# Performance work log

Measured on AMD Instinct MI355X. Metric: run time of the kernel, lower is better.

Reference implementation:

```python
import jax, jax.numpy as jnp
import numpy as np

N, DIM, HID, NCLS, E = 100000, 256, 16, 64, 3200000
NEG_SLOPE = 0.2


def setup_inputs() -> dict:
    key = jax.random.key(0)
    ks = jax.random.split(key, 10)
    x = jax.random.normal(ks[0], (N, DIM), dtype=jnp.float32)
    edge_index = jax.random.randint(ks[1], (2, E), 0, N, dtype=jnp.int64)
    # GATConv params (heads=1): glorot-ish scaled normals
    W1 = jax.random.normal(ks[2], (DIM, HID), dtype=jnp.float32) / np.sqrt(DIM)
    a_src1 = jax.random.normal(ks[3], (HID,), dtype=jnp.float32) / np.sqrt(HID)
    a_dst1 = jax.random.normal(ks[4], (HID,), dtype=jnp.float32) / np.sqrt(HID)
    b1 = jnp.zeros((HID,), dtype=jnp.float32)
    W2 = jax.random.normal(ks[5], (HID, NCLS), dtype=jnp.float32) / np.sqrt(HID)
    a_src2 = jax.random.normal(ks[6], (NCLS,), dtype=jnp.float32) / np.sqrt(NCLS)
    a_dst2 = jax.random.normal(ks[7], (NCLS,), dtype=jnp.float32) / np.sqrt(NCLS)
    b2 = jnp.zeros((NCLS,), dtype=jnp.float32)
    return {"x": x, "edge_index": edge_index, "W1": W1, "a_src1": a_src1,
            "a_dst1": a_dst1, "b1": b1, "W2": W2, "a_src2": a_src2,
            "a_dst2": a_dst2, "b2": b2}


def gat_conv(x, src, dst, W, a_s, a_d, b, n):
    # PyG GATConv, heads=1: h = x W; e_ij = LeakyReLU(a_s.h_j + a_d.h_i)
    h = x @ W                                   # [N, out]
    alpha_s = h @ a_s                           # [N]
    alpha_d = h @ a_d                           # [N]
    e = jax.nn.leaky_relu(alpha_s[src] + alpha_d[dst], NEG_SLOPE)  # [E]
    # softmax over edges grouped by destination node
    m = jax.ops.segment_max(e, dst, num_segments=n)
    m = jnp.where(jnp.isfinite(m), m, 0.0)
    ee = jnp.exp(e - m[dst])
    denom = jax.ops.segment_sum(ee, dst, num_segments=n)
    alpha = ee / denom[dst]                     # self-loops guarantee denom > 0
    out = jax.ops.segment_sum(h[src] * alpha[:, None], dst, num_segments=n)
    return out + b


def reference(x, edge_index, W1, a_src1, a_dst1, b1, W2, a_src2, a_dst2, b2):
    n = x.shape[0]
    loop = jnp.arange(n, dtype=edge_index.dtype)
    src = jnp.concatenate([edge_index[0], loop])  # add self-loops (PyG default)
    dst = jnp.concatenate([edge_index[1], loop])
    h = jax.nn.relu(gat_conv(x, src, dst, W1, a_src1, a_dst1, b1, n))
    # F.dropout treated as identity (inference / deterministic reference)
    out = gat_conv(h, src, dst, W2, a_src2, a_dst2, b2, n)
    return jax.nn.log_softmax(out, axis=1)
```

## Files before the change

kernel.cpp:

```cpp
#include <hip/hip_runtime.h>
#include <hip/hip_fp16.h>


#define DIM 256
#define HID 16
#define NCLS 64
#define NEG 0.2f
#define P1_CHUNK 4096
#define KITER 16
#define CAP 8704

typedef _Float16 f16x8 __attribute__((ext_vector_type(8)));
typedef float f32x4 __attribute__((ext_vector_type(4)));

__device__ __forceinline__ float lrelu(float v) { return v >= 0.f ? v : NEG * v; }

__device__ __forceinline__ uint4 pack_half8(const float* v) {
    __half2 p0 = __floats2half2_rn(v[0], v[1]);
    __half2 p1 = __floats2half2_rn(v[2], v[3]);
    __half2 p2 = __floats2half2_rn(v[4], v[5]);
    __half2 p3 = __floats2half2_rn(v[6], v[7]);
    return make_uint4(*(unsigned*)&p0, *(unsigned*)&p1, *(unsigned*)&p2, *(unsigned*)&p3);
}

__device__ __forceinline__ void unpack_half8(uint4 u, float* f) {
    float2 f0 = __half22float2(*(__half2*)&u.x);
    float2 f1 = __half22float2(*(__half2*)&u.y);
    float2 f2 = __half22float2(*(__half2*)&u.z);
    float2 f3 = __half22float2(*(__half2*)&u.w);
    f[0] = f0.x; f[1] = f0.y; f[2] = f1.x; f[3] = f1.y;
    f[4] = f2.x; f[5] = f2.y; f[6] = f3.x; f[7] = f3.y;
}

__global__ void vsd_kernel(const float* __restrict__ W2, const float* __restrict__ as2,
                           const float* __restrict__ ad2, float* __restrict__ vsd,
                           int* __restrict__ bkt_cnt, int* __restrict__ bkt_cur, int capb) {
    int t = threadIdx.x;
    bkt_cnt[t] = 0;
    bkt_cur[t] = capb ? t * capb : 0;
    if (t < 32) {
        int j = t & 15;
        const float* a = (t < 16) ? as2 : ad2;
        float s = 0.f;
        for (int c = 0; c < NCLS; ++c) s += W2[j * NCLS + c] * a[c];
        vsd[t] = s;
    }
}


__global__ __launch_bounds__(256) void p0_hist(const int* __restrict__ dst, int E,
                                               int* __restrict__ bkt_cnt) {
    __shared__ int hist[512];
    int t = threadIdx.x;
    for (int i = t; i < 512; i += 256) hist[i] = 0;
    __syncthreads();
    int base = blockIdx.x * P1_CHUNK;
#pragma unroll
    for (int k = 0; k < KITER; ++k) {
        int idx = base + k * 256 + t;
        if (idx < E) atomicAdd(&hist[dst[idx] >> 8], 1);
    }
    __syncthreads();
    for (int i = t; i < 512; i += 256)
        if (hist[i]) atomicAdd(&bkt_cnt[i], hist[i]);
}

__global__ void scanb(int* __restrict__ bkt_cnt, int* __restrict__ bkt_cur,
                      int* __restrict__ bkt_base, int nb) {
    __shared__ int lds[512];
    int t = threadIdx.x;
    int v = (t < nb) ? bkt_cnt[t] : 0;
    lds[t] = v;
    __syncthreads();
    for (int o = 1; o < 512; o <<= 1) {
        int x = (t >= o) ? lds[t - o] : 0;
        __syncthreads();
        lds[t] += x;
        __syncthreads();
    }
    if (t < nb) {
        int e = lds[t] - v;
        bkt_base[t] = e;
        bkt_cur[t] = e;
    }
}

struct H1S {
    _Float16 w1t[16][264];
    _Float16 hst[4][16][16];
};

__global__ __launch_bounds__(256) void p1h1_kernel(
    const int* __restrict__ ei, int E, int* __restrict__ bkt_cur,
    int* __restrict__ coarse, int nS, int h1blk, int capb,
    const float* __restrict__ x, const float* __restrict__ W1,
    uint4* __restrict__ h1h, int n) {
    __shared__ union __align__(16) { int hist[512]; H1S h1; } sm;
    int t = threadIdx.x;
    int bid = blockIdx.x;
    int total = nS + h1blk;
    int f0 = (int)(((long long)bid * h1blk) / total);
    int f1 = (int)(((long long)(bid + 1) * h1blk) / total);
    if (f1 == f0) {
        int sb = bid - f0;
        int base = sb * P1_CHUNK;
        int sarr[KITER], darr[KITER];
        for (int i = t; i < 512; i += 256) sm.hist[i] = 0;
        bool e4 = ((E & 3) == 0);
#pragma unroll
        for (int k = 0; k < KITER / 4; ++k) {
            int idx = base + (k * 256 + t) * 4;
            if (e4 && idx + 3 < E) {
                int4 s4 = *(const int4*)&ei[idx];
                int4 d4 = *(const int4*)&ei[E + idx];
                sarr[4 * k] = s4.x; sarr[4 * k + 1] = s4.y;
                sarr[4 * k + 2] = s4.z; sarr[4 * k + 3] = s4.w;
                darr[4 * k] = d4.x; darr[4 * k + 1] = d4.y;
                darr[4 * k + 2] = d4.z; darr[4 * k + 3] = d4.w;
            } else {
#pragma unroll
                for (int j = 0; j < 4; ++j) {
                    int id2 = idx + j;
                    if (id2 < E) { sarr[4 * k + j] = ei[id2]; darr[4 * k + j] = ei[E + id2]; }
                    else darr[4 * k + j] = -1;
                }
            }
        }
        __syncthreads();
#pragma unroll
        for (int k = 0; k < KITER; ++k)
            if (darr[k] >= 0) atomicAdd(&sm.hist[darr[k] >> 8], 1);
        __syncthreads();
        for (int b = t; b < 512; b += 256) {
            int c = sm.hist[b];
            sm.hist[b] = c ? atomicAdd(&bkt_cur[b], c) : 0;
        }
        __syncthreads();
#pragma unroll
        for (int k = 0; k < KITER; ++k) {
            int d = darr[k];
            if (d >= 0) {
                int bk = d >> 8;
                int pos = atomicAdd(&sm.hist[bk], 1);
                if (capb) pos = min(pos, (bk + 1) * capb - 1);
                coarse[pos] = (sarr[k] << 8) | (d & 255);
            }
        }
    } else {
        int hb = f0;
        {
            const float* row = W1 + t * HID;
#pragma unroll
            for (int nn2 = 0; nn2 < 16; ++nn2)
                sm.h1.w1t[nn2][t] = (_Float16)row[nn2];
        }
        __syncthreads();
        int lane = t & 63, wave = t >> 6;
        int q = lane >> 4, nn = lane & 15;
#pragma unroll 1
        for (int it = 0; it < 4; ++it) {
            int nb = hb * 256 + wave * 64 + it * 16;
            int node = nb + nn;
            const float* xr = x + (size_t)min(node, n - 1) * DIM;
            float4 st[16];
#pragma unroll
            for (int s = 0; s < 8; ++s) {
                int kb = s * 32 + q * 8;
                st[2 * s]     = *(const float4*)(xr + kb);
                st[2 * s + 1] = *(const float4*)(xr + kb + 4);
            }
            f32x4 acc = {0.f, 0.f, 0.f, 0.f};
#pragma unroll
            for (int s = 0; s < 8; ++s) {
                int kb = s * 32 + q * 8;
                f16x8 bf = *(const f16x8*)&sm.h1.w1t[nn][kb];
                float4 a0 = st[2 * s], a1 = st[2 * s + 1];
                f16x8 af;
                af[0] = (_Float16)a0.x; af[1] = (_Float16)a0.y;
                af[2] = (_Float16)a0.z; af[3] = (_Float16)a0.w;
                af[4] = (_Float16)a1.x; af[5] = (_Float16)a1.y;
                af[6] = (_Float16)a1.z; af[7] = (_Float16)a1.w;
                acc = __builtin_amdgcn_mfma_f32_16x16x32_f16(af, bf, acc, 0, 0, 0);
            }
            if (nb < n) {
#pragma unroll
                for (int r = 0; r < 4; ++r)
                    sm.h1.hst[wave][q * 4 + r][nn] = (_Float16)acc[r];
                __builtin_amdgcn_s_waitcnt(0);
                if (lane < 32) {
                    int nl = lane >> 1, jq = lane & 1;
                    int nd = nb + nl;
                    if (nd < n)
                        h1h[(size_t)nd * 2 + jq] = *(const uint4*)&sm.h1.hst[wave][nl][jq * 8];
                }
            }
        }
    }
}

__global__ __launch_bounds__(512) void p2_fine(const int* __restrict__ coarse,
                                               const int* __restrict__ bkt_base,
                                               const int* __restrict__ bkt_cnt,
                                               const int* __restrict__ bkt_cur,
                                               int* __restrict__ csr, int* __restrict__ row_ptr,
                                               int* __restrict__ deg, int n, int capb) {
    __shared__ int cnt[256];
    __shared__ int off[256];
    __shared__ int csr_loc[CAP];
    int b = blockIdx.x;
    int t = threadIdx.x;
    int m, wbase;
    if (capb) {
        int* sc = csr_loc;
        int cv = bkt_cur[t] - t * capb;
        sc[t] = cv;
        __syncthreads();
        for (int o = 1; o < 512; o <<= 1) {
            int xg = (t >= o) ? sc[t - o] : 0;
            __syncthreads();
            sc[t] += xg;
            __syncthreads();
        }
        m = bkt_cur[b] - b * capb;
        wbase = sc[b] - m;
        __syncthreads();
    } else {
        m = bkt_cnt[b];
        wbase = bkt_base[b];
    }
    int rbase = capb ? b * capb : wbase;
    if (t < 256) cnt[t] = 0;
    __syncthreads();
    for (int i = t; i < m; i += 512) atomicAdd(&cnt[coarse[rbase + i] & 255], 1);
    __syncthreads();
    int v = 0;
    if (t < 256) { v = cnt[t]; off[t] = v; }
    __syncthreads();
    for (int o = 1; o < 256; o <<= 1) {
        int xg = (t >= o && t < 256) ? off[t - o] : 0;
        __syncthreads();
        if (t < 256) off[t] += xg;
        __syncthreads();
    }
    if (t < 256) {
        int excl = off[t] - v;
        int node = b * 256 + t;
        if (node < n) {
            row_ptr[node] = wbase + excl;
            deg[node] = v;
        }
        cnt[t] = excl;
    }
    __syncthreads();
    if (m <= CAP) {
        for (int i = t; i < m; i += 512) {
            int rec = coarse[rbase + i];
            int pos = atomicAdd(&cnt[rec & 255], 1);
            csr_loc[pos] = rec >> 8;
        }
        __syncthreads();
        for (int i = t; i < m; i += 512) csr[wbase + i] = csr_loc[i];
    } else {
        for (int i = t; i < m; i += 512) {
            int rec = coarse[rbase + i];
            int pos = atomicAdd(&cnt[rec & 255], 1);
            csr[wbase + pos] = rec >> 8;
        }
    }
}


__device__ __forceinline__ void agg_core(
    const uint4* __restrict__ hh, const float* aw, const float* dw,
    int node, int start, int cnt, const int* __restrict__ csr,
    int lg, int eq, int jq, int gbase, float* acc, float* hs, float& denomv) {
    unpack_half8(hh[(size_t)node * 2 + jq], hs);
    float asn = 0.f, adn = 0.f;
#pragma unroll
    for (int i = 0; i < 8; ++i) { asn += hs[i] * aw[i]; adn += hs[i] * dw[i]; }
    asn += __shfl_xor(asn, 1, 64);
    adn += __shfl_xor(adn, 1, 64);
    float adi = adn;
    float w0 = __expf(lrelu(asn + adi));
    float w0s = (eq == 0) ? w0 : 0.f;
#pragma unroll
    for (int i = 0; i < 8; ++i) acc[i] = w0s * hs[i];
    float denom = w0s;
    int svA = (lg < cnt) ? csr[start + lg] : 0;
    int svB = (16 + lg < cnt) ? csr[start + 16 + lg] : 0;
#pragma unroll 1
    for (int q0 = 0; q0 < cnt; q0 += 32) {
        int nA = q0 + 32 + lg, nB = q0 + 48 + lg;
        int nsvA = (nA < cnt) ? csr[start + nA] : 0;
        int nsvB = (nB < cnt) ? csr[start + nB] : 0;
        int sl0 = gbase + eq, sl1 = gbase + 8 + eq;
        int s0 = __shfl(svA, sl0, 64);
        int s1 = __shfl(svA, sl1, 64);
        int s2 = __shfl(svB, sl0, 64);
        int s3 = __shfl(svB, sl1, 64);
        uint4 u0 = hh[(size_t)s0 * 2 + jq];
        uint4 u1 = hh[(size_t)s1 * 2 + jq];
        uint4 u2 = hh[(size_t)s2 * 2 + jq];
        uint4 u3 = hh[(size_t)s3 * 2 + jq];
        float h0[8], h1v[8], h2[8], h3[8];
        unpack_half8(u0, h0);
        unpack_half8(u1, h1v);
        unpack_half8(u2, h2);
        unpack_half8(u3, h3);
        float p0 = 0.f, p1 = 0.f, p2 = 0.f, p3 = 0.f;
#pragma unroll
        for (int i = 0; i < 8; ++i) {
            p0 += h0[i] * aw[i];
            p1 += h1v[i] * aw[i];
            p2 += h2[i] * aw[i];
            p3 += h3[i] * aw[i];
        }
        p0 += __shfl_xor(p0, 1, 64);
        p1 += __shfl_xor(p1, 1, 64);
        p2 += __shfl_xor(p2, 1, 64);
        p3 += __shfl_xor(p3, 1, 64);
        float wA = (q0 + eq < cnt)      ? __expf(lrelu(p0 + adi)) : 0.f;
        float wB = (q0 + 8 + eq < cnt)  ? __expf(lrelu(p1 + adi)) : 0.f;
        float wC = (q0 + 16 + eq < cnt) ? __expf(lrelu(p2 + adi)) : 0.f;
        float wD = (q0 + 24 + eq < cnt) ? __expf(lrelu(p3 + adi)) : 0.f;
        denom += wA + wB + wC + wD;
#pragma unroll
        for (int i = 0; i < 8; ++i)
            acc[i] += wA * h0[i] + wB * h1v[i] + wC * h2[i] + wD * h3[i];
        svA = nsvA;
        svB = nsvB;
    }
#pragma unroll
    for (int m = 2; m <= 8; m <<= 1) {
#pragma unroll
        for (int i = 0; i < 8; ++i) acc[i] += __shfl_xor(acc[i], m, 64);
        denom += __shfl_xor(denom, m, 64);
    }
    denomv = denom;
}

__global__ __launch_bounds__(256) void agg1_kernel(
    const uint4* __restrict__ hh,
    const int* __restrict__ row_ptr, const int* __restrict__ deg, const int* __restrict__ csr,
    const float* __restrict__ as1, const float* __restrict__ ad1,
    const float* __restrict__ bias, uint4* __restrict__ outh, int n) {
    int t = threadIdx.x;
    int node = blockIdx.x * 16 + (t >> 4);
    if (node >= n) return;
    int lg = t & 15, jq = lg & 1, eq = lg >> 1, gbase = t & 48;
    float aw[8], dw[8];
#pragma unroll
    for (int i = 0; i < 8; ++i) { aw[i] = as1[jq * 8 + i]; dw[i] = ad1[jq * 8 + i]; }
    float acc[8], hs[8];
    float denom;
    agg_core(hh, aw, dw, node, row_ptr[node], deg[node], csr, lg, eq, jq, gbase, acc, hs, denom);
    float inv = 1.f / denom;
    float val[8];
#pragma unroll
    for (int i = 0; i < 8; ++i) val[i] = fmaxf(acc[i] * inv + bias[jq * 8 + i], 0.f);
    if (eq == 0) outh[(size_t)node * 2 + jq] = pack_half8(val);
}

__global__ __launch_bounds__(256) void agg2_final_kernel(
    const uint4* __restrict__ hh,
    const int* __restrict__ row_ptr, const int* __restrict__ deg, const int* __restrict__ csr,
    const float* __restrict__ vsd,
    const float* __restrict__ W2, const float* __restrict__ b2,
    float* __restrict__ out, int n) {
    __shared__ float a2s[16 * HID];
    __shared__ float w2s[HID * NCLS];
    __shared__ float b2s[NCLS];
    int t = threadIdx.x;
    for (int i = t; i < HID * NCLS; i += 256) w2s[i] = W2[i];
    if (t < NCLS) b2s[t] = b2[t];
    int g = t >> 4;
    int node = blockIdx.x * 16 + g;
    int lg = t & 15, jq = lg & 1, eq = lg >> 1, gbase = t & 48;
    if (node < n) {
        float aw[8], dw[8];
#pragma unroll
        for (int i = 0; i < 8; ++i) { aw[i] = vsd[jq * 8 + i]; dw[i] = vsd[16 + jq * 8 + i]; }
        float acc[8], hs[8];
        float denom;
        agg_core(hh, aw, dw, node, row_ptr[node], deg[node], csr, lg, eq, jq, gbase, acc, hs, denom);
        float inv = 1.f / denom;
        if (eq == 0) {
            float* dst = &a2s[g * HID + jq * 8];
            *(float4*)dst = make_float4(acc[0] * inv, acc[1] * inv, acc[2] * inv, acc[3] * inv);
            *(float4*)(dst + 4) = make_float4(acc[4] * inv, acc[5] * inv, acc[6] * inv, acc[7] * inv);
        }
    }
    __syncthreads();
    int wv = t >> 6;
    int c = t & 63;
#pragma unroll
    for (int i = 0; i < 4; ++i) {
        int nl = i * 4 + wv;
        int gn = blockIdx.x * 16 + nl;
        if (gn >= n) continue;
        const float* ar = &a2s[nl * HID];
        float v = b2s[c];
#pragma unroll
        for (int j = 0; j < HID; ++j) v += ar[j] * w2s[j * NCLS + c];
        float mx = v;
#pragma unroll
        for (int off = 1; off < 64; off <<= 1) mx = fmaxf(mx, __shfl_xor(mx, off, 64));
        float ex = __expf(v - mx);
        float s = ex;
#pragma unroll
        for (int off = 1; off < 64; off <<= 1) s += __shfl_xor(s, off, 64);
        out[(size_t)gn * NCLS + c] = (v - mx) - __logf(s);
    }
}

extern "C" void kernel_launch(void* const* d_in, const int* in_sizes, int n_in,
                              void* d_out, int out_size, void* d_ws, size_t ws_size,
                              hipStream_t stream) {
    const float* x    = (const float*)d_in[0];
    const int*   ei   = (const int*)d_in[1];
    const float* W1   = (const float*)d_in[2];
    const float* a_s1 = (const float*)d_in[3];
    const float* a_d1 = (const float*)d_in[4];
    const float* b1   = (const float*)d_in[5];
    const float* W2   = (const float*)d_in[6];
    const float* a_s2 = (const float*)d_in[7];
    const float* a_d2 = (const float*)d_in[8];
    const float* b2   = (const float*)d_in[9];
    float* out = (float*)d_out;

    const int N = in_sizes[0] / DIM;
    const int E = in_sizes[1] / 2;
    const int NB = (N + 255) >> 8;
    const int nS = (E + P1_CHUNK - 1) / P1_CHUNK;
    const int h1blk = (N + 255) / 256;

    char* p = (char*)d_ws;
    auto alloc = [&](size_t bytes) {
        char* r = p;
        p += (bytes + 255) & ~(size_t)255;
        return r;
    };
    int*   bkt_cnt  = (int*)alloc(512 * 4);
    int*   bkt_base = (int*)alloc(512 * 4);
    int*   bkt_cur  = (int*)alloc(512 * 4);
    int*   csr      = (int*)alloc((size_t)E * 4);
    int*   row_ptr  = (int*)alloc((size_t)N * 4);
    int*   deg      = (int*)alloc((size_t)N * 4);
    float* vsd      = (float*)alloc(32 * 4);
    uint4* h1h      = (uint4*)alloc((size_t)N * 32);
    uint4* hreluh   = (uint4*)alloc((size_t)N * 32);

    int capb = 10240;
    size_t used = (size_t)(p - (char*)d_ws);
    size_t pad_bytes = (size_t)512 * capb * 4;
    int* coarse;
    if (ws_size - used >= pad_bytes) {
        coarse = (int*)alloc(pad_bytes);
    } else {
        capb = 0;
        coarse = (int*)alloc((size_t)E * 4);
    }

    vsd_kernel<<<1, 512, 0, stream>>>(W2, a_s2, a_d2, vsd, bkt_cnt, bkt_cur, capb);
    if (!capb) {
        p0_hist<<<nS, 256, 0, stream>>>(ei + E, E, bkt_cnt);
        scanb<<<1, 512, 0, stream>>>(bkt_cnt, bkt_cur, bkt_base, NB);
    }
    p1h1_kernel<<<nS + h1blk, 256, 0, stream>>>(ei, E, bkt_cur, coarse, nS, h1blk, capb,
                                                x, W1, h1h, N);
    p2_fine<<<NB, 512, 0, stream>>>(coarse, bkt_base, bkt_cnt, bkt_cur,
                                    csr, row_ptr, deg, N, capb);
    agg1_kernel<<<(N + 15) / 16, 256, 0, stream>>>(h1h, row_ptr, deg, csr,
                                                   a_s1, a_d1, b1, hreluh, N);
    agg2_final_kernel<<<(N + 15) / 16, 256, 0, stream>>>(hreluh, row_ptr, deg, csr,
                                                         vsd, W2, b2, out, N);
}
```

Measured before the change: 299.8 us.

## Drop fine CSR build; aggregate edges per coarse bucket with shared-memory atomics

Removes the p2_fine pass that turned coarse 256-node buckets into a full CSR. Instead, each 512-thread block walks its bucket's edge list directly and accumulates softmax-weighted neighbour features and denominators into shared memory with atomics. It skips the per-node max subtraction and adds the self-loop term at the end. This saves one kernel and the CSR write/read traffic, but uses only about 391 blocks, depends heavily on LDS float atomics (17 per edge), and drops the max-stabilisation, so exp could overflow on other inputs.

```diff
diff --git a/kernel.cpp b/kernel.cpp
--- a/kernel.cpp
+++ b/kernel.cpp
@@ -8,7 +8,6 @@
 #define NEG 0.2f
 #define P1_CHUNK 4096
 #define KITER 16
-#define CAP 8704
 
 typedef _Float16 f16x8 __attribute__((ext_vector_type(8)));
 typedef float f32x4 __attribute__((ext_vector_type(4)));
@@ -30,6 +29,13 @@
     float2 f3 = __half22float2(*(__half2*)&u.w);
     f[0] = f0.x; f[1] = f0.y; f[2] = f1.x; f[3] = f1.y;
     f[4] = f2.x; f[5] = f2.y; f[6] = f3.x; f[7] = f3.y;
+}
+
+__device__ __forceinline__ void unpack_row(const uint4* __restrict__ hh, int s, float* h) {
+    uint4 u0 = hh[(size_t)s * 2];
+    uint4 u1 = hh[(size_t)s * 2 + 1];
+    unpack_half8(u0, h);
+    unpack_half8(u1, h + 8);
 }
 
 __global__ void vsd_kernel(const float* __restrict__ W2, const float* __restrict__ as2,
@@ -198,218 +204,215 @@
     }
 }
 
-__global__ __launch_bounds__(512) void p2_fine(const int* __restrict__ coarse,
-                                               const int* __restrict__ bkt_base,
-                                               const int* __restrict__ bkt_cnt,
-                                               const int* __restrict__ bkt_cur,
-                                               int* __restrict__ csr, int* __restrict__ row_ptr,
-                                               int* __restrict__ deg, int n, int capb) {
-    __shared__ int cnt[256];
-    __shared__ int off[256];
-    __shared__ int csr_loc[CAP];
+
+__global__ __launch_bounds__(512) void agg1_edge_kernel(
+    const int* __restrict__ coarse, const int* __restrict__ bkt_base,
+    const int* __restrict__ bkt_cnt, const int* __restrict__ bkt_cur, int capb,
+    const uint4* __restrict__ hh, const float* __restrict__ a_s1,
+    const float* __restrict__ a_d1, const float* __restrict__ b1,
+    uint4* __restrict__ outh, int n) {
+    __shared__ float acc[256][17];
+    __shared__ float denom[256];
+    __shared__ float asl[256];
+    __shared__ float adl[256];
+    __shared__ float aswv[16], adwv[16], b1s[16];
     int b = blockIdx.x;
     int t = threadIdx.x;
-    int m, wbase;
-    if (capb) {
-        int* sc = csr_loc;
-        int cv = bkt_cur[t] - t * capb;
-        sc[t] = cv;
-        __syncthreads();
-        for (int o = 1; o < 512; o <<= 1) {
-            int xg = (t >= o) ? sc[t - o] : 0;
-            __syncthreads();
-            sc[t] += xg;
-            __syncthreads();
-        }
-        m = bkt_cur[b] - b * capb;
-        wbase = sc[b] - m;
-        __syncthreads();
-    } else {
-        m = bkt_cnt[b];
-        wbase = bkt_base[b];
-    }
-    int rbase = capb ? b * capb : wbase;
-    if (t < 256) cnt[t] = 0;
-    __syncthreads();
-    for (int i = t; i < m; i += 512) atomicAdd(&cnt[coarse[rbase + i] & 255], 1);
-    __syncthreads();
-    int v = 0;
-    if (t < 256) { v = cnt[t]; off[t] = v; }
-    __syncthreads();
-    for (int o = 1; o < 256; o <<= 1) {
-        int xg = (t >= o && t < 256) ? off[t - o] : 0;
-        __syncthreads();
-        if (t < 256) off[t] += xg;
-        __syncthreads();
-    }
+    if (t < 16) { aswv[t] = a_s1[t]; adwv[t] = a_d1[t]; b1s[t] = b1[t]; }
+    for (int i = t; i < 256 * 17; i += 512) ((float*)acc)[i] = 0.f;
+    if (t < 256) denom[t] = 0.f;
+    __syncthreads();
     if (t < 256) {
-        int excl = off[t] - v;
+        int node = b * 256 + t;
+        float s1 = 0.f, s2 = 0.f;
+        if (node < n) {
+            float h[16];
+            unpack_row(hh, node, h);
+#pragma unroll
+            for (int j = 0; j < 16; ++j) { s1 += h[j] * aswv[j]; s2 += h[j] * adwv[j]; }
+        }
+        asl[t] = s1;
+        adl[t] = s2;
+    }
+    __syncthreads();
+    int rb, m;
+    if (capb) { rb = b * capb; m = bkt_cur[b] - rb; }
+    else { rb = bkt_base[b]; m = bkt_cnt[b]; }
+    int i = t;
+    while (i + 512 < m) {
+        int r0 = coarse[rb + i];
+        int r1 = coarse[rb + i + 512];
+        int s0 = r0 >> 8, d0 = r0 & 255;
+        int s1v = r1 >> 8, d1v = r1 & 255;
+        float h0[16], h1[16];
+        unpack_row(hh, s0, h0);
+        unpack_row(hh, s1v, h1);
+        float p0 = 0.f, p1 = 0.f;
+#pragma unroll
+        for (int j = 0; j < 16; ++j) { p0 += h0[j] * aswv[j]; p1 += h1[j] * aswv[j]; }
+        float w0 = __expf(lrelu(p0 + adl[d0]));
+        float w1 = __expf(lrelu(p1 + adl[d1v]));
+#pragma unroll
+        for (int j = 0; j < 16; ++j) {
+            atomicAdd(&acc[d0][j], w0 * h0[j]);
+            atomicAdd(&acc[d1v][j], w1 * h1[j]);
+        }
+        atomicAdd(&denom[d0], w0);
+        atomicAdd(&denom[d1v], w1);
+        i += 1024;
+    }
+    while (i < m) {
+        int r0 = coarse[rb + i];
+        int s0 = r0 >> 8, d0 = r0 & 255;
+        float h0[16];
+        unpack_row(hh, s0, h0);
+        float p0 = 0.f;
+#pragma unroll
+        for (int j = 0; j < 16; ++j) p0 += h0[j] * aswv[j];
+        float w0 = __expf(lrelu(p0 + adl[d0]));
+#pragma unroll
+        for (int j = 0; j < 16; ++j) atomicAdd(&acc[d0][j], w0 * h0[j]);
+        atomicAdd(&denom[d0], w0);
+        i += 512;
+    }
+    __syncthreads();
+    if (t < 256) {
         int node = b * 256 + t;
         if (node < n) {
-            row_ptr[node] = wbase + excl;
-            deg[node] = v;
-        }
-        cnt[t] = excl;
-    }
-    __syncthreads();
-    if (m <= CAP) {
-        for (int i = t; i < m; i += 512) {
-            int rec = coarse[rbase + i];
-            int pos = atomicAdd(&cnt[rec & 255], 1);
-            csr_loc[pos] = rec >> 8;
-        }
-        __syncthreads();
-        for (int i = t; i < m; i += 512) csr[wbase + i] = csr_loc[i];
-    } else {
-        for (int i = t; i < m; i += 512) {
-            int rec = coarse[rbase + i];
-            int pos = atomicAdd(&cnt[rec & 255], 1);
-            csr[wbase + pos] = rec >> 8;
-        }
-    }
-}
-
-
-__device__ __forceinline__ void agg_core(
-    const uint4* __restrict__ hh, const float* aw, const float* dw,
-    int node, int start, int cnt, const int* __restrict__ csr,
-    int lg, int eq, int jq, int gbase, float* acc, float* hs, float& denomv) {
-    unpack_half8(hh[(size_t)node * 2 + jq], hs);
-    float asn = 0.f, adn = 0.f;
-#pragma unroll
-    for (int i = 0; i < 8; ++i) { asn += hs[i] * aw[i]; adn += hs[i] * dw[i]; }
-    asn += __shfl_xor(asn, 1, 64);
-    adn += __shfl_xor(adn, 1, 64);
-    float adi = adn;
-    float w0 = __expf(lrelu(asn + adi));
-    float w0s = (eq == 0) ? w0 : 0.f;
-#pragma unroll
-    for (int i = 0; i < 8; ++i) acc[i] = w0s * hs[i];
-    float denom = w0s;
-    int svA = (lg < cnt) ? csr[start + lg] : 0;
-    int svB = (16 + lg < cnt) ? csr[start + 16 + lg] : 0;
-#pragma unroll 1
-    for (int q0 = 0; q0 < cnt; q0 += 32) {
-        int nA = q0 + 32 + lg, nB = q0 + 48 + lg;
-        int nsvA = (nA < cnt) ? csr[start + nA] : 0;
-        int nsvB = (nB < cnt) ? csr[start + nB] : 0;
-        int sl0 = gbase + eq, sl1 = gbase + 8 + eq;
-        int s0 = __shfl(svA, sl0, 64);
-        int s1 = __shfl(svA, sl1, 64);
-        int s2 = __shfl(svB, sl0, 64);
-        int s3 = __shfl(svB, sl1, 64);
-        uint4 u0 = hh[(size_t)s0 * 2 + jq];
-        uint4 u1 = hh[(size_t)s1 * 2 + jq];
-        uint4 u2 = hh[(size_t)s2 * 2 + jq];
-        uint4 u3 = hh[(size_t)s3 * 2 + jq];
-        float h0[8], h1v[8], h2[8], h3[8];
-        unpack_half8(u0, h0);
-        unpack_half8(u1, h1v);
-        unpack_half8(u2, h2);
-        unpack_half8(u3, h3);
-        float p0 = 0.f, p1 = 0.f, p2 = 0.f, p3 = 0.f;
-#pragma unroll
-        for (int i = 0; i < 8; ++i) {
-            p0 += h0[i] * aw[i];
-            p1 += h1v[i] * aw[i];
-            p2 += h2[i] * aw[i];
-            p3 += h3[i] * aw[i];
-        }
-        p0 += __shfl_xor(p0, 1, 64);
-        p1 += __shfl_xor(p1, 1, 64);
-        p2 += __shfl_xor(p2, 1, 64);
-        p3 += __shfl_xor(p3, 1, 64);
-        float wA = (q0 + eq < cnt)      ? __expf(lrelu(p0 + adi)) : 0.f;
-        float wB = (q0 + 8 + eq < cnt)  ? __expf(lrelu(p1 + adi)) : 0.f;
-        float wC = (q0 + 16 + eq < cnt) ? __expf(lrelu(p2 + adi)) : 0.f;
-        float wD = (q0 + 24 + eq < cnt) ? __expf(lrelu(p3 + adi)) : 0.f;
-        denom += wA + wB + wC + wD;
-#pragma unroll
-        for (int i = 0; i < 8; ++i)
-            acc[i] += wA * h0[i] + wB * h1v[i] + wC * h2[i] + wD * h3[i];
-        svA = nsvA;
-        svB = nsvB;
-    }
-#pragma unroll
-    for (int m = 2; m <= 8; m <<= 1) {
-#pragma unroll
-        for (int i = 0; i < 8; ++i) acc[i] += __shfl_xor(acc[i], m, 64);
-        denom += __shfl_xor(denom, m, 64);
-    }
-    denomv = denom;
-}
-
-__global__ __launch_bounds__(256) void agg1_kernel(
-    const uint4* __restrict__ hh,
-    const int* __restrict__ row_ptr, const int* __restrict__ deg, const int* __restrict__ csr,
-    const float* __restrict__ as1, const float* __restrict__ ad1,
-    const float* __restrict__ bias, uint4* __restrict__ outh, int n) {
-    int t = threadIdx.x;
-    int node = blockIdx.x * 16 + (t >> 4);
-    if (node >= n) return;
-    int lg = t & 15, jq = lg & 1, eq = lg >> 1, gbase = t & 48;
-    float aw[8], dw[8];
-#pragma unroll
-    for (int i = 0; i < 8; ++i) { aw[i] = as1[jq * 8 + i]; dw[i] = ad1[jq * 8 + i]; }
-    float acc[8], hs[8];
-    float denom;
-    agg_core(hh, aw, dw, node, row_ptr[node], deg[node], csr, lg, eq, jq, gbase, acc, hs, denom);
-    float inv = 1.f / denom;
-    float val[8];
-#pragma unroll
-    for (int i = 0; i < 8; ++i) val[i] = fmaxf(acc[i] * inv + bias[jq * 8 + i], 0.f);
-    if (eq == 0) outh[(size_t)node * 2 + jq] = pack_half8(val);
-}
-
-__global__ __launch_bounds__(256) void agg2_final_kernel(
-    const uint4* __restrict__ hh,
-    const int* __restrict__ row_ptr, const int* __restrict__ deg, const int* __restrict__ csr,
-    const float* __restrict__ vsd,
+            float h[16];
+            unpack_row(hh, node, h);
+            float w0 = __expf(lrelu(asl[t] + adl[t]));
+            float inv = 1.f / (denom[t] + w0);
+            float val[16];
+#pragma unroll
+            for (int j = 0; j < 16; ++j)
+                val[j] = fmaxf((acc[t][j] + w0 * h[j]) * inv + b1s[j], 0.f);
+            outh[(size_t)node * 2]     = pack_half8(val);
+            outh[(size_t)node * 2 + 1] = pack_half8(val + 8);
+        }
+    }
+}
+
+
+__global__ __launch_bounds__(512) void agg2_edge_kernel(
+    const int* __restrict__ coarse, const int* __restrict__ bkt_base,
+    const int* __restrict__ bkt_cnt, const int* __restrict__ bkt_cur, int capb,
+    const uint4* __restrict__ hh, const float* __restrict__ vsd,
     const float* __restrict__ W2, const float* __restrict__ b2,
     float* __restrict__ out, int n) {
-    __shared__ float a2s[16 * HID];
+    __shared__ float acc[256][17];
+    __shared__ float denom[256];
+    __shared__ float asl[256];
+    __shared__ float adl[256];
+    __shared__ float vs[16], vd[16];
     __shared__ float w2s[HID * NCLS];
     __shared__ float b2s[NCLS];
-    int t = threadIdx.x;
-    for (int i = t; i < HID * NCLS; i += 256) w2s[i] = W2[i];
+    int b = blockIdx.x;
+    int t = threadIdx.x;
+    if (t < 16) { vs[t] = vsd[t]; vd[t] = vsd[16 + t]; }
     if (t < NCLS) b2s[t] = b2[t];
-    int g = t >> 4;
-    int node = blockIdx.x * 16 + g;
-    int lg = t & 15, jq = lg & 1, eq = lg >> 1, gbase = t & 48;
-    if (node < n) {
-        float aw[8], dw[8];
-#pragma unroll
-        for (int i = 0; i < 8; ++i) { aw[i] = vsd[jq * 8 + i]; dw[i] = vsd[16 + jq * 8 + i]; }
-        float acc[8], hs[8];
-        float denom;
-        agg_core(hh, aw, dw, node, row_ptr[node], deg[node], csr, lg, eq, jq, gbase, acc, hs, denom);
-        float inv = 1.f / denom;
-        if (eq == 0) {
-            float* dst = &a2s[g * HID + jq * 8];
-            *(float4*)dst = make_float4(acc[0] * inv, acc[1] * inv, acc[2] * inv, acc[3] * inv);
-            *(float4*)(dst + 4) = make_float4(acc[4] * inv, acc[5] * inv, acc[6] * inv, acc[7] * inv);
-        }
-    }
-    __syncthreads();
-    int wv = t >> 6;
-    int c = t & 63;
-#pragma unroll
-    for (int i = 0; i < 4; ++i) {
-        int nl = i * 4 + wv;
-        int gn = blockIdx.x * 16 + nl;
-        if (gn >= n) continue;
-        const float* ar = &a2s[nl * HID];
-        float v = b2s[c];
-#pragma unroll
-        for (int j = 0; j < HID; ++j) v += ar[j] * w2s[j * NCLS + c];
-        float mx = v;
-#pragma unroll
-        for (int off = 1; off < 64; off <<= 1) mx = fmaxf(mx, __shfl_xor(mx, off, 64));
-        float ex = __expf(v - mx);
-        float s = ex;
-#pragma unroll
-        for (int off = 1; off < 64; off <<= 1) s += __shfl_xor(s, off, 64);
-        out[(size_t)gn * NCLS + c] = (v - mx) - __logf(s);
+    for (int i = t; i < HID * NCLS; i += 512) w2s[i] = W2[i];
+    for (int i = t; i < 256 * 17; i += 512) ((float*)acc)[i] = 0.f;
+    if (t < 256) denom[t] = 0.f;
+    __syncthreads();
+    if (t < 256) {
+        int node = b * 256 + t;
+        float s1 = 0.f, s2 = 0.f;
+        if (node < n) {
+            float h[16];
+            unpack_row(hh, node, h);
+#pragma unroll
+            for (int j = 0; j < 16; ++j) { s1 += h[j] * vs[j]; s2 += h[j] * vd[j]; }
+        }
+        asl[t] = s1;
+        adl[t] = s2;
+    }
+    __syncthreads();
+    int rb, m;
+    if (capb) { rb = b * capb; m = bkt_cur[b] - rb; }
+    else { rb = bkt_base[b]; m = bkt_cnt[b]; }
+    int i = t;
+    while (i + 512 < m) {
+        int r0 = coarse[rb + i];
+        int r1 = coarse[rb + i + 512];
+        int s0 = r0 >> 8, d0 = r0 & 255;
+        int s1v = r1 >> 8, d1v = r1 & 255;
+        float h0[16], h1[16];
+        unpack_row(hh, s0, h0);
+        unpack_row(hh, s1v, h1);
+        float p0 = 0.f, p1 = 0.f;
+#pragma unroll
+        for (int j = 0; j < 16; ++j) { p0 += h0[j] * vs[j]; p1 += h1[j] * vs[j]; }
+        float w0 = __expf(lrelu(p0 + adl[d0]));
+        float w1 = __expf(lrelu(p1 + adl[d1v]));
+#pragma unroll
+        for (int j = 0; j < 16; ++j) {
+            atomicAdd(&acc[d0][j], w0 * h0[j]);
+            atomicAdd(&acc[d1v][j], w1 * h1[j]);
+        }
+        atomicAdd(&denom[d0], w0);
+        atomicAdd(&denom[d1v], w1);
+        i += 1024;
+    }
+    while (i < m) {
+        int r0 = coarse[rb + i];
+        int s0 = r0 >> 8, d0 = r0 & 255;
+        float h0[16];
+        unpack_row(hh, s0, h0);
+        float p0 = 0.f;
+#pragma unroll
+        for (int j = 0; j < 16; ++j) p0 += h0[j] * vs[j];
+        float w0 = __expf(lrelu(p0 + adl[d0]));
+#pragma unroll
+        for (int j = 0; j < 16; ++j) atomicAdd(&acc[d0][j], w0 * h0[j]);
+        atomicAdd(&denom[d0], w0);
+        i += 512;
+    }
+    __syncthreads();
+    if (t < 256) {
+        int node = b * 256 + t;
+        if (node < n) {
+            float h[16];
+            unpack_row(hh, node, h);
+            float w0 = __expf(lrelu(asl[t] + adl[t]));
+            float inv = 1.f / (denom[t] + w0);
+#pragma unroll
+            for (int j = 0; j < 16; ++j)
+                acc[t][j] = (acc[t][j] + w0 * h[j]) * inv;
+        }
+    }
+    __syncthreads();
+    int lane8 = t & 7;
+#pragma unroll 1
+    for (int pass = 0; pass < 4; ++pass) {
+        int nl = pass * 64 + (t >> 3);
+        int node = b * 256 + nl;
+        if (node < n) {
+            const float* ar = acc[nl];
+            float v[8];
+#pragma unroll
+            for (int c8 = 0; c8 < 8; ++c8) {
+                int c = lane8 * 8 + c8;
+                float s = b2s[c];
+#pragma unroll
+                for (int j = 0; j < HID; ++j) s += ar[j] * w2s[j * NCLS + c];
+                v[c8] = s;
+            }
+            float mx = v[0];
+#pragma unroll
+            for (int c8 = 1; c8 < 8; ++c8) mx = fmaxf(mx, v[c8]);
+#pragma unroll
+            for (int off = 1; off < 8; off <<= 1) mx = fmaxf(mx, __shfl_xor(mx, off, 64));
+            float s = 0.f;
+#pragma unroll
+            for (int c8 = 0; c8 < 8; ++c8) s += __expf(v[c8] - mx);
+#pragma unroll
+            for (int off = 1; off < 8; off <<= 1) s += __shfl_xor(s, off, 64);
+            float lg = __logf(s);
+            float* orow = out + (size_t)node * NCLS + lane8 * 8;
+#pragma unroll
+            for (int c8 = 0; c8 < 8; ++c8) orow[c8] = (v[c8] - mx) - lg;
+        }
     }
 }
 
@@ -443,9 +446,6 @@
     int*   bkt_cnt  = (int*)alloc(512 * 4);
     int*   bkt_base = (int*)alloc(512 * 4);
     int*   bkt_cur  = (int*)alloc(512 * 4);
-    int*   csr      = (int*)alloc((size_t)E * 4);
-    int*   row_ptr  = (int*)alloc((size_t)N * 4);
-    int*   deg      = (int*)alloc((size_t)N * 4);
     float* vsd      = (float*)alloc(32 * 4);
     uint4* h1h      = (uint4*)alloc((size_t)N * 32);
     uint4* hreluh   = (uint4*)alloc((size_t)N * 32);
@@ -468,10 +468,8 @@
     }
     p1h1_kernel<<<nS + h1blk, 256, 0, stream>>>(ei, E, bkt_cur, coarse, nS, h1blk, capb,
                                                 x, W1, h1h, N);
-    p2_fine<<<NB, 512, 0, stream>>>(coarse, bkt_base, bkt_cnt, bkt_cur,
-                                    csr, row_ptr, deg, N, capb);
-    agg1_kernel<<<(N + 15) / 16, 256, 0, stream>>>(h1h, row_ptr, deg, csr,
-                                                   a_s1, a_d1, b1, hreluh, N);
-    agg2_final_kernel<<<(N + 15) / 16, 256, 0, stream>>>(hreluh, row_ptr, deg, csr,
-                                                         vsd, W2, b2, out, N);
-}
+    agg1_edge_kernel<<<NB, 512, 0, stream>>>(coarse, bkt_base, bkt_cnt, bkt_cur, capb,
+                                             h1h, a_s1, a_d1, b1, hreluh, N);
+    agg2_edge_kernel<<<NB, 512, 0, stream>>>(coarse, bkt_base, bkt_cnt, bkt_cur, capb,
+                                             hreluh, vsd, W2, b2, out, N);
+}
```

Result: slower. 933.6 us (+211.3%).

## Stream x rows into LDS with async global_load_lds and widen p2_fine blocks

Applied to the files above, without the earlier changes.

The h1 projection now loads x rows straight into a per-wave LDS ring buffer using global_load_lds, with a swizzled layout and staged vmcnt waits. This lets later k-slices stream in while MFMAs run on earlier ones, replacing the register-staged float4 loads. Separately, the fine CSR bucketing kernel moves from 512 to 1024 threads per block, with guards so the 512-entry scan still uses only the first 512 threads. The hand-written waitcnt sequencing is fragile, and the extra LDS buffer may cut occupancy of the fused p1/h1 kernel.

```diff
diff --git a/kernel.cpp b/kernel.cpp
--- a/kernel.cpp
+++ b/kernel.cpp
@@ -12,6 +12,12 @@
 
 typedef _Float16 f16x8 __attribute__((ext_vector_type(8)));
 typedef float f32x4 __attribute__((ext_vector_type(4)));
+
+typedef const __attribute__((address_space(1))) void gas_void;
+typedef __attribute__((address_space(3))) void las_void;
+__device__ __forceinline__ void gload_lds16(const void* g, void* l) {
+    __builtin_amdgcn_global_load_lds((gas_void*)g, (las_void*)l, 16, 0, 0);
+}
 
 __device__ __forceinline__ float lrelu(float v) { return v >= 0.f ? v : NEG * v; }
 
@@ -96,6 +102,7 @@
     const float* __restrict__ x, const float* __restrict__ W1,
     uint4* __restrict__ h1h, int n) {
     __shared__ union __align__(16) { int hist[512]; H1S h1; } sm;
+    __shared__ float xbuf[4][4][2][16][16];
     int t = threadIdx.x;
     int bid = blockIdx.x;
     int total = nS + h1blk;
@@ -157,36 +164,49 @@
         __syncthreads();
         int lane = t & 63, wave = t >> 6;
         int q = lane >> 4, nn = lane & 15;
+        int ln = lane >> 2, scn = lane & 3, cc = (scn - ln) & 3;
 #pragma unroll 1
         for (int it = 0; it < 4; ++it) {
             int nb = hb * 256 + wave * 64 + it * 16;
-            int node = nb + nn;
-            const float* xr = x + (size_t)min(node, n - 1) * DIM;
-            float4 st[16];
-#pragma unroll
-            for (int s = 0; s < 8; ++s) {
-                int kb = s * 32 + q * 8;
-                st[2 * s]     = *(const float4*)(xr + kb);
-                st[2 * s + 1] = *(const float4*)(xr + kb + 4);
+            const float* gb = x + (size_t)min(nb + ln, n - 1) * DIM + cc * 4;
+#pragma unroll
+            for (int k = 0; k < 4; ++k) {
+                gload_lds16(gb + k * 32,      &xbuf[wave][k][0][0][0]);
+                gload_lds16(gb + k * 32 + 16, &xbuf[wave][k][1][0][0]);
             }
             f32x4 acc = {0.f, 0.f, 0.f, 0.f};
 #pragma unroll
             for (int s = 0; s < 8; ++s) {
-                int kb = s * 32 + q * 8;
-                f16x8 bf = *(const f16x8*)&sm.h1.w1t[nn][kb];
-                float4 a0 = st[2 * s], a1 = st[2 * s + 1];
+                int rem = 7 - s;
+                int wn = (rem > 3 ? 3 : rem) * 2;
+                if (wn == 6)      asm volatile("s_waitcnt vmcnt(6)" ::: "memory");
+                else if (wn == 4) asm volatile("s_waitcnt vmcnt(4)" ::: "memory");
+                else if (wn == 2) asm volatile("s_waitcnt vmcnt(2)" ::: "memory");
+                else              asm volatile("s_waitcnt vmcnt(0)" ::: "memory");
+                int slot = s & 3;
+                int z = q >> 1;
+                int c1 = (2 * q) & 3;
+                int s1 = (c1 + nn) & 3, s2 = (c1 + 1 + nn) & 3;
+                float4 a0 = *(const float4*)&xbuf[wave][slot][z][nn][s1 * 4];
+                float4 a1 = *(const float4*)&xbuf[wave][slot][z][nn][s2 * 4];
+                f16x8 bf = *(const f16x8*)&sm.h1.w1t[nn][s * 32 + q * 8];
                 f16x8 af;
                 af[0] = (_Float16)a0.x; af[1] = (_Float16)a0.y;
                 af[2] = (_Float16)a0.z; af[3] = (_Float16)a0.w;
                 af[4] = (_Float16)a1.x; af[5] = (_Float16)a1.y;
                 af[6] = (_Float16)a1.z; af[7] = (_Float16)a1.w;
+                if (s + 4 < 8) {
+                    asm volatile("s_waitcnt lgkmcnt(0)" ::: "memory");
+                    gload_lds16(gb + (s + 4) * 32,      &xbuf[wave][slot][0][0][0]);
+                    gload_lds16(gb + (s + 4) * 32 + 16, &xbuf[wave][slot][1][0][0]);
+                }
                 acc = __builtin_amdgcn_mfma_f32_16x16x32_f16(af, bf, acc, 0, 0, 0);
             }
             if (nb < n) {
 #pragma unroll
                 for (int r = 0; r < 4; ++r)
                     sm.h1.hst[wave][q * 4 + r][nn] = (_Float16)acc[r];
-                __builtin_amdgcn_s_waitcnt(0);
+                asm volatile("s_waitcnt lgkmcnt(0)" ::: "memory");
                 if (lane < 32) {
                     int nl = lane >> 1, jq = lane & 1;
                     int nd = nb + nl;
@@ -198,12 +218,12 @@
     }
 }
 
-__global__ __launch_bounds__(512) void p2_fine(const int* __restrict__ coarse,
-                                               const int* __restrict__ bkt_base,
-                                               const int* __restrict__ bkt_cnt,
-                                               const int* __restrict__ bkt_cur,
-                                               int* __restrict__ csr, int* __restrict__ row_ptr,
-                                               int* __restrict__ deg, int n, int capb) {
+__global__ __launch_bounds__(1024) void p2_fine(const int* __restrict__ coarse,
+                                                const int* __restrict__ bkt_base,
+                                                const int* __restrict__ bkt_cnt,
+                                                const int* __restrict__ bkt_cur,
+                                                int* __restrict__ csr, int* __restrict__ row_ptr,
+                                                int* __restrict__ deg, int n, int capb) {
     __shared__ int cnt[256];
     __shared__ int off[256];
     __shared__ int csr_loc[CAP];
@@ -212,13 +232,12 @@
     int m, wbase;
     if (capb) {
         int* sc = csr_loc;
-        int cv = bkt_cur[t] - t * capb;
-        sc[t] = cv;
+        if (t < 512) sc[t] = bkt_cur[t] - t * capb;
         __syncthreads();
         for (int o = 1; o < 512; o <<= 1) {
-            int xg = (t >= o) ? sc[t - o] : 0;
+            int xg = (t >= o && t < 512) ? sc[t - o] : 0;
             __syncthreads();
-            sc[t] += xg;
+            if (t < 512) sc[t] += xg;
             __syncthreads();
         }
         m = bkt_cur[b] - b * capb;
@@ -231,7 +250,7 @@
     int rbase = capb ? b * capb : wbase;
     if (t < 256) cnt[t] = 0;
     __syncthreads();
-    for (int i = t; i < m; i += 512) atomicAdd(&cnt[coarse[rbase + i] & 255], 1);
+    for (int i = t; i < m; i += 1024) atomicAdd(&cnt[coarse[rbase + i] & 255], 1);
     __syncthreads();
     int v = 0;
     if (t < 256) { v = cnt[t]; off[t] = v; }
@@ -253,15 +272,15 @@
     }
     __syncthreads();
     if (m <= CAP) {
-        for (int i = t; i < m; i += 512) {
+        for (int i = t; i < m; i += 1024) {
             int rec = coarse[rbase + i];
             int pos = atomicAdd(&cnt[rec & 255], 1);
             csr_loc[pos] = rec >> 8;
         }
         __syncthreads();
-        for (int i = t; i < m; i += 512) csr[wbase + i] = csr_loc[i];
+        for (int i = t; i < m; i += 1024) csr[wbase + i] = csr_loc[i];
     } else {
-        for (int i = t; i < m; i += 512) {
+        for (int i = t; i < m; i += 1024) {
             int rec = coarse[rbase + i];
             int pos = atomicAdd(&cnt[rec & 255], 1);
             csr[wbase + pos] = rec >> 8;
@@ -468,8 +487,8 @@
     }
     p1h1_kernel<<<nS + h1blk, 256, 0, stream>>>(ei, E, bkt_cur, coarse, nS, h1blk, capb,
                                                 x, W1, h1h, N);
-    p2_fine<<<NB, 512, 0, stream>>>(coarse, bkt_base, bkt_cnt, bkt_cur,
-                                    csr, row_ptr, deg, N, capb);
+    p2_fine<<<NB, 1024, 0, stream>>>(coarse, bkt_base, bkt_cnt, bkt_cur,
+                                     csr, row_ptr, deg, N, capb);
     agg1_kernel<<<(N + 15) / 16, 256, 0, stream>>>(h1h, row_ptr, deg, csr,
                                                    a_s1, a_d1, b1, hreluh, N);
     agg2_final_kernel<<<(N + 15) / 16, 256, 0, stream>>>(hreluh, row_ptr, deg, csr,
```

Result: no change. 304.5 us (+1.5%).

## Software-pipeline neighbor gathers in aggregation and widen CSR fine-sort blocks

Applied to the files above, without the earlier changes.

The aggregation core now issues the csr index loads and fp16 feature gathers for the next 32 edges one iteration ahead, replacing the prefetch-plus-shuffle scheme. Loads now come directly per lane, and out-of-range lanes fall back to the node itself to keep addresses valid. The per-edge work is processed one gather at a time to reduce live registers. Separately, the fine bucketing kernel runs 1024 threads per block instead of 512, with the scan guarded to the first 512 threads. This raises register pressure from the held-in-flight loads and adds redundant csr loads per lane, in exchange for more memory-level parallelism.

```diff
diff --git a/kernel.cpp b/kernel.cpp
--- a/kernel.cpp
+++ b/kernel.cpp
@@ -198,12 +198,12 @@
     }
 }
 
-__global__ __launch_bounds__(512) void p2_fine(const int* __restrict__ coarse,
-                                               const int* __restrict__ bkt_base,
-                                               const int* __restrict__ bkt_cnt,
-                                               const int* __restrict__ bkt_cur,
-                                               int* __restrict__ csr, int* __restrict__ row_ptr,
-                                               int* __restrict__ deg, int n, int capb) {
+__global__ __launch_bounds__(1024) void p2_fine(const int* __restrict__ coarse,
+                                                const int* __restrict__ bkt_base,
+                                                const int* __restrict__ bkt_cnt,
+                                                const int* __restrict__ bkt_cur,
+                                                int* __restrict__ csr, int* __restrict__ row_ptr,
+                                                int* __restrict__ deg, int n, int capb) {
     __shared__ int cnt[256];
     __shared__ int off[256];
     __shared__ int csr_loc[CAP];
@@ -212,13 +212,12 @@
     int m, wbase;
     if (capb) {
         int* sc = csr_loc;
-        int cv = bkt_cur[t] - t * capb;
-        sc[t] = cv;
+        if (t < 512) sc[t] = bkt_cur[t] - t * capb;
         __syncthreads();
         for (int o = 1; o < 512; o <<= 1) {
-            int xg = (t >= o) ? sc[t - o] : 0;
+            int xg = (t >= o && t < 512) ? sc[t - o] : 0;
             __syncthreads();
-            sc[t] += xg;
+            if (t < 512) sc[t] += xg;
             __syncthreads();
         }
         m = bkt_cur[b] - b * capb;
@@ -231,7 +230,7 @@
     int rbase = capb ? b * capb : wbase;
     if (t < 256) cnt[t] = 0;
     __syncthreads();
-    for (int i = t; i < m; i += 512) atomicAdd(&cnt[coarse[rbase + i] & 255], 1);
+    for (int i = t; i < m; i += 1024) atomicAdd(&cnt[coarse[rbase + i] & 255], 1);
     __syncthreads();
     int v = 0;
     if (t < 256) { v = cnt[t]; off[t] = v; }
@@ -253,15 +252,15 @@
     }
     __syncthreads();
     if (m <= CAP) {
-        for (int i = t; i < m; i += 512) {
+        for (int i = t; i < m; i += 1024) {
             int rec = coarse[rbase + i];
             int pos = atomicAdd(&cnt[rec & 255], 1);
             csr_loc[pos] = rec >> 8;
         }
         __syncthreads();
-        for (int i = t; i < m; i += 512) csr[wbase + i] = csr_loc[i];
+        for (int i = t; i < m; i += 1024) csr[wbase + i] = csr_loc[i];
     } else {
-        for (int i = t; i < m; i += 512) {
+        for (int i = t; i < m; i += 1024) {
             int rec = coarse[rbase + i];
             int pos = atomicAdd(&cnt[rec & 255], 1);
             csr[wbase + pos] = rec >> 8;
@@ -273,7 +272,7 @@
 __device__ __forceinline__ void agg_core(
     const uint4* __restrict__ hh, const float* aw, const float* dw,
     int node, int start, int cnt, const int* __restrict__ csr,
-    int lg, int eq, int jq, int gbase, float* acc, float* hs, float& denomv) {
+    int eq, int jq, float* acc, float* hs, float& denomv) {
     unpack_half8(hh[(size_t)node * 2 + jq], hs);
     float asn = 0.f, adn = 0.f;
 #pragma unroll
@@ -286,49 +285,63 @@
 #pragma unroll
     for (int i = 0; i < 8; ++i) acc[i] = w0s * hs[i];
     float denom = w0s;
-    int svA = (lg < cnt) ? csr[start + lg] : 0;
-    int svB = (16 + lg < cnt) ? csr[start + 16 + lg] : 0;
+    int s0 = (eq < cnt)      ? csr[start + eq]      : node;
+    int s1 = (8 + eq < cnt)  ? csr[start + 8 + eq]  : node;
+    int s2 = (16 + eq < cnt) ? csr[start + 16 + eq] : node;
+    int s3 = (24 + eq < cnt) ? csr[start + 24 + eq] : node;
+    uint4 u0 = hh[(size_t)s0 * 2 + jq];
+    uint4 u1 = hh[(size_t)s1 * 2 + jq];
+    uint4 u2 = hh[(size_t)s2 * 2 + jq];
+    uint4 u3 = hh[(size_t)s3 * 2 + jq];
 #pragma unroll 1
     for (int q0 = 0; q0 < cnt; q0 += 32) {
-        int nA = q0 + 32 + lg, nB = q0 + 48 + lg;
-        int nsvA = (nA < cnt) ? csr[start + nA] : 0;
-        int nsvB = (nB < cnt) ? csr[start + nB] : 0;
-        int sl0 = gbase + eq, sl1 = gbase + 8 + eq;
-        int s0 = __shfl(svA, sl0, 64);
-        int s1 = __shfl(svA, sl1, 64);
-        int s2 = __shfl(svB, sl0, 64);
-        int s3 = __shfl(svB, sl1, 64);
-        uint4 u0 = hh[(size_t)s0 * 2 + jq];
-        uint4 u1 = hh[(size_t)s1 * 2 + jq];
-        uint4 u2 = hh[(size_t)s2 * 2 + jq];
-        uint4 u3 = hh[(size_t)s3 * 2 + jq];
-        float h0[8], h1v[8], h2[8], h3[8];
-        unpack_half8(u0, h0);
-        unpack_half8(u1, h1v);
-        unpack_half8(u2, h2);
-        unpack_half8(u3, h3);
-        float p0 = 0.f, p1 = 0.f, p2 = 0.f, p3 = 0.f;
-#pragma unroll
-        for (int i = 0; i < 8; ++i) {
-            p0 += h0[i] * aw[i];
-            p1 += h1v[i] * aw[i];
-            p2 += h2[i] * aw[i];
-            p3 += h3[i] * aw[i];
-        }
-        p0 += __shfl_xor(p0, 1, 64);
-        p1 += __shfl_xor(p1, 1, 64);
-        p2 += __shfl_xor(p2, 1, 64);
-        p3 += __shfl_xor(p3, 1, 64);
-        float wA = (q0 + eq < cnt)      ? __expf(lrelu(p0 + adi)) : 0.f;
-        float wB = (q0 + 8 + eq < cnt)  ? __expf(lrelu(p1 + adi)) : 0.f;
-        float wC = (q0 + 16 + eq < cnt) ? __expf(lrelu(p2 + adi)) : 0.f;
-        float wD = (q0 + 24 + eq < cnt) ? __expf(lrelu(p3 + adi)) : 0.f;
-        denom += wA + wB + wC + wD;
-#pragma unroll
-        for (int i = 0; i < 8; ++i)
-            acc[i] += wA * h0[i] + wB * h1v[i] + wC * h2[i] + wD * h3[i];
-        svA = nsvA;
-        svB = nsvB;
+        int nq = q0 + 32;
+        int t0 = (nq + eq < cnt)      ? csr[start + nq + eq]      : node;
+        int t1 = (nq + 8 + eq < cnt)  ? csr[start + nq + 8 + eq]  : node;
+        int t2 = (nq + 16 + eq < cnt) ? csr[start + nq + 16 + eq] : node;
+        int t3 = (nq + 24 + eq < cnt) ? csr[start + nq + 24 + eq] : node;
+        uint4 v0 = hh[(size_t)t0 * 2 + jq];
+        uint4 v1 = hh[(size_t)t1 * 2 + jq];
+        uint4 v2 = hh[(size_t)t2 * 2 + jq];
+        uint4 v3 = hh[(size_t)t3 * 2 + jq];
+        float h[8], p, wv;
+        unpack_half8(u0, h);
+        p = 0.f;
+#pragma unroll
+        for (int i = 0; i < 8; ++i) p += h[i] * aw[i];
+        p += __shfl_xor(p, 1, 64);
+        wv = (q0 + eq < cnt) ? __expf(lrelu(p + adi)) : 0.f;
+        denom += wv;
+#pragma unroll
+        for (int i = 0; i < 8; ++i) acc[i] += wv * h[i];
+        unpack_half8(u1, h);
+        p = 0.f;
+#pragma unroll
+        for (int i = 0; i < 8; ++i) p += h[i] * aw[i];
+        p += __shfl_xor(p, 1, 64);
+        wv = (q0 + 8 + eq < cnt) ? __expf(lrelu(p + adi)) : 0.f;
+        denom += wv;
+#pragma unroll
+        for (int i = 0; i < 8; ++i) acc[i] += wv * h[i];
+        unpack_half8(u2, h);
+        p = 0.f;
+#pragma unroll
+        for (int i = 0; i < 8; ++i) p += h[i] * aw[i];
+        p += __shfl_xor(p, 1, 64);
+        wv = (q0 + 16 + eq < cnt) ? __expf(lrelu(p + adi)) : 0.f;
+        denom += wv;
+#pragma unroll
+        for (int i = 0; i < 8; ++i) acc[i] += wv * h[i];
+        unpack_half8(u3, h);
+        p = 0.f;
+#pragma unroll
+        for (int i = 0; i < 8; ++i) p += h[i] * aw[i];
+        p += __shfl_xor(p, 1, 64);
+        wv = (q0 + 24 + eq < cnt) ? __expf(lrelu(p + adi)) : 0.f;
+        denom += wv;
+#pragma unroll
+        for (int i = 0; i < 8; ++i) acc[i] += wv * h[i];
+        u0 = v0; u1 = v1; u2 = v2; u3 = v3;
     }
 #pragma unroll
     for (int m = 2; m <= 8; m <<= 1) {
@@ -347,13 +360,13 @@
     int t = threadIdx.x;
     int node = blockIdx.x * 16 + (t >> 4);
     if (node >= n) return;
-    int lg = t & 15, jq = lg & 1, eq = lg >> 1, gbase = t & 48;
+    int lg = t & 15, jq = lg & 1, eq = lg >> 1;
     float aw[8], dw[8];
 #pragma unroll
     for (int i = 0; i < 8; ++i) { aw[i] = as1[jq * 8 + i]; dw[i] = ad1[jq * 8 + i]; }
     float acc[8], hs[8];
     float denom;
-    agg_core(hh, aw, dw, node, row_ptr[node], deg[node], csr, lg, eq, jq, gbase, acc, hs, denom);
+    agg_core(hh, aw, dw, node, row_ptr[node], deg[node], csr, eq, jq, acc, hs, denom);
     float inv = 1.f / denom;
     float val[8];
 #pragma unroll
@@ -375,14 +388,14 @@
     if (t < NCLS) b2s[t] = b2[t];
     int g = t >> 4;
     int node = blockIdx.x * 16 + g;
-    int lg = t & 15, jq = lg & 1, eq = lg >> 1, gbase = t & 48;
+    int lg = t & 15, jq = lg & 1, eq = lg >> 1;
     if (node < n) {
         float aw[8], dw[8];
 #pragma unroll
         for (int i = 0; i < 8; ++i) { aw[i] = vsd[jq * 8 + i]; dw[i] = vsd[16 + jq * 8 + i]; }
         float acc[8], hs[8];
         float denom;
-        agg_core(hh, aw, dw, node, row_ptr[node], deg[node], csr, lg, eq, jq, gbase, acc, hs, denom);
+        agg_core(hh, aw, dw, node, row_ptr[node], deg[node], csr, eq, jq, acc, hs, denom);
         float inv = 1.f / denom;
         if (eq == 0) {
             float* dst = &a2s[g * HID + jq * 8];
@@ -468,8 +481,8 @@
     }
     p1h1_kernel<<<nS + h1blk, 256, 0, stream>>>(ei, E, bkt_cur, coarse, nS, h1blk, capb,
                                                 x, W1, h1h, N);
-    p2_fine<<<NB, 512, 0, stream>>>(coarse, bkt_base, bkt_cnt, bkt_cur,
-                                    csr, row_ptr, deg, N, capb);
+    p2_fine<<<NB, 1024, 0, stream>>>(coarse, bkt_base, bkt_cnt, bkt_cur,
+                                     csr, row_ptr, deg, N, capb);
     agg1_kernel<<<(N + 15) / 16, 256, 0, stream>>>(h1h, row_ptr, deg, csr,
                                                    a_s1, a_d1, b1, hreluh, N);
     agg2_final_kernel<<<(N + 15) / 16, 256, 0, stream>>>(hreluh, row_ptr, deg, csr,
```

Result: faster. 289.2 us (-3.6%).
